# Kernel optimization log

Measured on AMD Instinct MI355X. Metric: run time of the kernel, lower is better.

## Reference

```python
import jax, jax.numpy as jnp
import numpy as np

IN_DIM = 128
LAYER_DIMS = [128, 128]
NUM_SAMPLES = [25, 10]
L0 = 3072
NEG_WEIGHT = 1.0


def setup_inputs() -> dict:
    key = jax.random.key(0)
    ks = jax.random.split(key, 12)
    feat = jax.random.normal(ks[0], (L0, IN_DIM), dtype=jnp.float32)
    nodes = jax.random.randint(ks[1], (L0,), 0, L0)
    nb0 = jnp.arange(L0)
    nb1 = jax.random.randint(ks[2], (L0 * 10,), 0, L0)
    nb2 = jax.random.randint(ks[3], (L0 * 10 * 25,), 0, L0)
    src_idx = jax.random.randint(ks[4], (1024,), 0, L0)
    pos_idx = jax.random.randint(ks[5], (1024,), 0, L0)
    neg_idx = jax.random.randint(ks[6], (512,), 0, L0)
    g = 0.05
    # mean aggregator weights: layer0 in=IN_DIM, layer1 in=2*128 (concat)
    w_self_0 = jax.random.normal(ks[7], (IN_DIM, 128), jnp.float32) * g
    w_neigh_0 = jax.random.normal(ks[8], (IN_DIM, 128), jnp.float32) * g
    w_self_1 = jax.random.normal(ks[9], (256, 128), jnp.float32) * g
    w_neigh_1 = jax.random.normal(ks[10], (256, 128), jnp.float32) * g
    return dict(nodes=nodes, feat=feat, src_idx=src_idx, pos_idx=pos_idx,
                neg_idx=neg_idx, nb0=nb0, nb1=nb1, nb2=nb2,
                w_self_0=w_self_0, w_neigh_0=w_neigh_0,
                w_self_1=w_self_1, w_neigh_1=w_neigh_1)


def _aggregate(hidden, params):
    # GraphSAGE layer stack: at layer l, combine each hop with the mean of its
    # sampled neighbors, concat self/neigh transforms, relu except last layer.
    num_layers = len(NUM_SAMPLES)
    for layer in range(num_layers):
        w_self, w_neigh = params[layer]
        is_last = layer == num_layers - 1
        next_hidden = []
        for hop in range(num_layers - layer):
            s = NUM_SAMPLES[num_layers - hop - 1]
            self_v = hidden[hop]  # [n, d]
            neigh = hidden[hop + 1].reshape(self_v.shape[0], s, self_v.shape[1])
            neigh_mean = jnp.mean(neigh, axis=1)
            h = jnp.concatenate([self_v @ w_self, neigh_mean @ w_neigh], axis=1)
            if not is_last:
                h = jax.nn.relu(h)
            next_hidden.append(h)
        hidden = next_hidden
    return hidden[0]


def _l2_normalize(x, eps=1e-12):
    return x * jax.lax.rsqrt(jnp.maximum(jnp.sum(x * x, axis=1, keepdims=True), eps))


def reference(nodes, feat, src_idx, pos_idx, neg_idx, nb0, nb1, nb2,
              w_self_0, w_neigh_0, w_self_1, w_neigh_1):
    hidden = [feat[nb0], feat[nb1], feat[nb2]]
    params = [(w_self_0, w_neigh_0), (w_self_1, w_neigh_1)]
    output = _aggregate(hidden, params)          # [L0, 256]
    output = _l2_normalize(output)
    src_emb = output[src_idx]                    # [B, 256]
    pos_emb = output[pos_idx]
    neg_emb = output[neg_idx]                    # [Nneg, 256]

    aff = jnp.sum(src_emb * pos_emb, axis=1)     # [B]
    neg_aff = src_emb @ neg_emb.T                # [B, Nneg]

    # MRR via double argsort (tf double top_k equivalent; ties -> positive last)
    aff_all = jnp.concatenate([neg_aff, aff[:, None]], axis=1)
    order = jnp.argsort(-aff_all, axis=1, stable=True)
    ranks = jnp.argsort(order, axis=1, stable=True)
    mrr = jnp.mean(1.0 / (ranks[:, -1].astype(jnp.float32) + 1.0))

    # sigmoid cross-entropy: labels 1 -> softplus(-x); labels 0 -> softplus(x)
    true_xent = jax.nn.softplus(-aff)
    neg_xent = jax.nn.softplus(neg_aff)
    loss = jnp.sum(true_xent) + NEG_WEIGHT * jnp.sum(neg_xent)
    loss = loss / jnp.asarray(src_emb.shape[0], jnp.float32)
    return src_emb, loss, mrr
```

## Files before the change

kernel.cpp:

```cpp
#include <hip/hip_runtime.h>
#include <math.h>

#define L0      3072
#define BATCH   1024
#define NNEG    512
#define LDP     264

typedef __attribute__((ext_vector_type(8))) short bf16x8;
typedef __attribute__((ext_vector_type(4))) float f32x4;


__device__ __forceinline__ float bf2f(unsigned short u) {
  return __uint_as_float(((unsigned)u) << 16);
}
__device__ __forceinline__ void store_out(float v, float* p) { *p = v; }
__device__ __forceinline__ void store_out(float v, unsigned short* p) {
  unsigned x = __float_as_uint(v);
  *p = (unsigned short)((x + 0x7fff + ((x >> 16) & 1)) >> 16);
}

template<int K, int AW, int HOFF, bool NORM, typename OutT>
__global__ __launch_bounds__(512) void k_mm(
    const float* __restrict__ Ain,
    const float* __restrict__ W0, const float* __restrict__ W1,
    OutT* __restrict__ Out, const int ldo, const int outHalfOff,
    unsigned short* __restrict__ OutB,
    float* __restrict__ zbuf, const int zcount) {
  __shared__ float AT[6 * AW];
  __shared__ float rs[8][3];
  const int t = threadIdx.x;
  if (zbuf != nullptr && blockIdx.x == 0)
    for (int z = t; z < zcount; z += 512) zbuf[z] = 0.f;
  const int base = blockIdx.x * 6;
  {
    const float4* __restrict__ src = (const float4*)(Ain + base * AW);
    float4* __restrict__ dst = (float4*)AT;
    for (int idx = t; idx < 6 * AW / 4; idx += 512) dst[idx] = src[idx];
  }
  __syncthreads();

  const int wave = t >> 6;
  const int half = wave >> 2;
  const int colg = (wave >> 1) & 1;
  const int rowg = wave & 1;
  const int rg = rowg * 3;
  const int col = colg * 64 + (t & 63);
  const float* __restrict__ W = (half ? W1 : W0) + col;
  const float* __restrict__ A0 = AT + rg * AW + half * HOFF;

  float acc[3] = {0.f, 0.f, 0.f};
#pragma unroll 4
  for (int d = 0; d < K; d += 4) {
    float4 a[3];
#pragma unroll
    for (int r = 0; r < 3; ++r) a[r] = *(const float4*)&A0[r * AW + d];
    float w[4];
#pragma unroll
    for (int i2 = 0; i2 < 4; ++i2) w[i2] = W[(d + i2) * 128];
#pragma unroll
    for (int i2 = 0; i2 < 4; ++i2)
#pragma unroll
      for (int r = 0; r < 3; ++r)
        acc[r] = fmaf(((const float*)&a[r])[i2], w[i2], acc[r]);
  }

  float scale[3] = {1.f, 1.f, 1.f};
  if (NORM) {
    float p[3];
#pragma unroll
    for (int r = 0; r < 3; ++r) p[r] = acc[r] * acc[r];
#pragma unroll
    for (int off = 32; off > 0; off >>= 1)
#pragma unroll
      for (int r = 0; r < 3; ++r) p[r] += __shfl_xor(p[r], off, 64);
    if ((t & 63) == 0) { rs[wave][0] = p[0]; rs[wave][1] = p[1]; rs[wave][2] = p[2]; }
    __syncthreads();
#pragma unroll
    for (int r = 0; r < 3; ++r) {
      const float s = rs[rowg][r] + rs[rowg + 2][r] + rs[rowg + 4][r] + rs[rowg + 6][r];
      scale[r] = rsqrtf(fmaxf(s, 1e-12f));
    }
  }
  OutT* __restrict__ O = Out + half * outHalfOff;
#pragma unroll
  for (int r = 0; r < 3; ++r) {
    const float v = acc[r] * scale[r];
    store_out(v, &O[(base + rg + r) * ldo + col]);
    if (OutB != nullptr)
      store_out(v, &OutB[(base + rg + r) * 256 + half * 128 + col]);
  }
}

__global__ __launch_bounds__(640) void k_aggregate(
    const unsigned short* __restrict__ X0, const unsigned short* __restrict__ Y0,
    const int* __restrict__ nb0, const int* __restrict__ nb1,
    const int* __restrict__ nb2, float* __restrict__ H) {
  __shared__ float gB[10][128], gC[10][128], gD[10][128];
  const int i = blockIdx.x;
  const int t = threadIdx.x;
  const int n0 = nb0[i];
  const int j = t >> 6;
  const int lam = t & 63;
  const int r = i * 10 + j;
  int myidx = 0;
  if (lam < 25) myidx = nb2[r * 25 + lam];
  else if (lam == 25) myidx = nb1[r];
  const int c8 = lam & 15;
  const int sub = lam >> 4;

  float d8[8];
#pragma unroll
  for (int e = 0; e < 8; ++e) d8[e] = 0.f;
#pragma unroll
  for (int m = 0; m < 7; ++m) {
    const int k = sub + 4 * m;
    const int ridx = __shfl(myidx, k, 64);
    if (k < 25) {
      const float4 raw = *(const float4*)(Y0 + ridx * 128 + c8 * 8);
      const unsigned short* u = (const unsigned short*)&raw;
#pragma unroll
      for (int e = 0; e < 8; ++e) d8[e] += bf2f(u[e]);
    }
  }
#pragma unroll
  for (int e = 0; e < 8; ++e) d8[e] += __shfl_xor(d8[e], 16, 64);
#pragma unroll
  for (int e = 0; e < 8; ++e) d8[e] += __shfl_xor(d8[e], 32, 64);

  const int r1 = __shfl(myidx, 25, 64);
  if (sub == 0) {
#pragma unroll
    for (int e = 0; e < 8; ++e) gD[j][c8 * 8 + e] = fmaxf(d8[e] * 0.04f, 0.f);
    const float4 raw = *(const float4*)(Y0 + r1 * 128 + c8 * 8);
    const unsigned short* u = (const unsigned short*)&raw;
#pragma unroll
    for (int e = 0; e < 8; ++e) gB[j][c8 * 8 + e] = bf2f(u[e]);
  } else if (sub == 1) {
    const float4 raw = *(const float4*)(X0 + r1 * 128 + c8 * 8);
    const unsigned short* u = (const unsigned short*)&raw;
#pragma unroll
    for (int e = 0; e < 8; ++e) gC[j][c8 * 8 + e] = fmaxf(bf2f(u[e]), 0.f);
  }
  __syncthreads();

  if (t < 512) {
    const int q = t >> 7, c = t & 127;
    float v;
    if (q == 0) {
      v = fmaxf(bf2f(X0[n0 * 128 + c]), 0.f);
    } else {
      const float* g = (q == 1) ? &gB[0][0] : (q == 2) ? &gC[0][0] : &gD[0][0];
      float s = 0.f;
#pragma unroll
      for (int jj = 0; jj < 10; ++jj) s += g[jj * 128 + c];
      v = s * 0.1f;
      if (q == 1) v = fmaxf(v, 0.f);
    }
    H[i * 512 + t] = v;
  }
}

__device__ __forceinline__ float softplusf(float x) {
  return fmaxf(x, 0.f) + log1pf(expf(-fabsf(x)));
}

__global__ __launch_bounds__(64) void k_aff(
    const unsigned short* __restrict__ Rb, const float* __restrict__ R,
    const int* __restrict__ src_idx, const int* __restrict__ pos_idx,
    float* __restrict__ out_src, float* __restrict__ aff,
    float* __restrict__ spPos) {
  __shared__ unsigned short Sb[16][LDP];
  __shared__ unsigned short Pb[16][LDP];
  const int t = threadIdx.x;
  const int rowBase = blockIdx.x * 16;
  for (int idx = t; idx < 32 * 32; idx += 64) {
    const int row = idx >> 5, q = idx & 31;
    const int gr = (row < 16) ? src_idx[rowBase + row] : pos_idx[rowBase + row - 16];
    const float4 v = ((const float4*)(Rb + gr * 256))[q];
    unsigned short* dst = (row < 16) ? &Sb[row][0] : &Pb[row - 16][0];
    *(float4*)(dst + q * 8) = v;
  }
  for (int idx = t; idx < 16 * 64; idx += 64) {
    const int row = idx >> 6, q = idx & 63;
    ((float4*)out_src)[(rowBase + row) * 64 + q] =
        ((const float4*)(R + src_idx[rowBase + row] * 256))[q];
  }
  __syncthreads();
  const int lm = t & 15, quad = t >> 4;
  const unsigned short* Sp = &Sb[lm][quad * 8];
  const unsigned short* Pp = &Pb[lm][quad * 8];
  f32x4 d = {0.f, 0.f, 0.f, 0.f};
#pragma unroll
  for (int k0 = 0; k0 < 256; k0 += 32) {
    bf16x8 a = *(const bf16x8*)(Sp + k0);
    bf16x8 b = *(const bf16x8*)(Pp + k0);
    d = __builtin_amdgcn_mfma_f32_16x16x32_bf16(a, b, d, 0, 0, 0);
  }
#pragma unroll
  for (int j = 0; j < 4; ++j) {
    const int row = quad * 4 + j;
    if (lm == row) {
      aff[rowBase + row] = d[j];
      atomicAdd(spPos, softplusf(-d[j]));
    }
  }
}

__global__ __launch_bounds__(256) void k_neg(
    const unsigned short* __restrict__ Rb, const int* __restrict__ src_idx,
    const int* __restrict__ neg_idx, const float* __restrict__ aff,
    int* __restrict__ rank, float* __restrict__ spNeg) {
  __shared__ unsigned short Sb[32][LDP];
  __shared__ unsigned short Nb[64][LDP];
  __shared__ float affL[32];
  const int t = threadIdx.x;
  const int rowBase = (blockIdx.x >> 3) * 32;
  const int colBase = (blockIdx.x & 7) * 64;
  if (t < 32) affL[t] = aff[rowBase + t];
  for (int idx = t; idx < 96 * 32; idx += 256) {
    const int row = idx >> 5, q = idx & 31;
    const int gr = (row < 32) ? src_idx[rowBase + row]
                              : neg_idx[colBase + row - 32];
    const float4 v = ((const float4*)(Rb + gr * 256))[q];
    unsigned short* dst = (row < 32) ? &Sb[row][0] : &Nb[row - 32][0];
    *(float4*)(dst + q * 8) = v;
  }
  __syncthreads();

  const int l = t & 63, w = t >> 6;
  const int mt = w & 1, np = w >> 1;
  const int lm = l & 15, quad = l >> 4;
  const unsigned short* Sp = &Sb[mt * 16 + lm][quad * 8];
  const unsigned short* N0 = &Nb[np * 32 + lm][quad * 8];
  const unsigned short* N1 = &Nb[np * 32 + 16 + lm][quad * 8];
  f32x4 d0 = {0.f, 0.f, 0.f, 0.f}, d1 = {0.f, 0.f, 0.f, 0.f};
#pragma unroll
  for (int k0 = 0; k0 < 256; k0 += 32) {
    bf16x8 a = *(const bf16x8*)(Sp + k0);
    bf16x8 b0 = *(const bf16x8*)(N0 + k0);
    bf16x8 b1 = *(const bf16x8*)(N1 + k0);
    d0 = __builtin_amdgcn_mfma_f32_16x16x32_bf16(a, b0, d0, 0, 0, 0);
    d1 = __builtin_amdgcn_mfma_f32_16x16x32_bf16(a, b1, d1, 0, 0, 0);
  }

  float sp = 0.f;
#pragma unroll
  for (int j = 0; j < 4; ++j) {
    const int row = mt * 16 + quad * 4 + j;
    const float a = affL[row];
    const float v0 = d0[j], v1 = d1[j];
    sp += softplusf(v0) + softplusf(v1);
    int c = (v0 >= a ? 1 : 0) + (v1 >= a ? 1 : 0);
#pragma unroll
    for (int off = 8; off > 0; off >>= 1) c += __shfl_down(c, off, 16);
    if (lm == 0 && c) atomicAdd(&rank[rowBase + row], c);
  }
#pragma unroll
  for (int off = 32; off > 0; off >>= 1) sp += __shfl_down(sp, off, 64);
  if (l == 0) atomicAdd(spNeg, sp);
}

__global__ __launch_bounds__(256) void k_finalize(
    const int* __restrict__ rank, const float* __restrict__ spPos,
    const float* __restrict__ spNeg, float* __restrict__ out) {
  const int t = threadIdx.x;
  float s = 0.f;
  for (int i = t; i < BATCH; i += 256) s += 1.f / (float)(rank[i] + 1);
#pragma unroll
  for (int off = 32; off > 0; off >>= 1) s += __shfl_down(s, off, 64);
  __shared__ float wsum[4];
  if ((t & 63) == 0) wsum[t >> 6] = s;
  __syncthreads();
  if (t == 0) {
    float mrr = (wsum[0] + wsum[1] + wsum[2] + wsum[3]) * (1.f / 1024.f);
    float loss = (spPos[0] + spNeg[0]) * (1.f / 1024.f);
    out[BATCH * 256]     = loss;
    out[BATCH * 256 + 1] = mrr;
  }
}

extern "C" void kernel_launch(void* const* d_in, const int* in_sizes, int n_in,
                              void* d_out, int out_size, void* d_ws, size_t ws_size,
                              hipStream_t stream) {
  const float* feat   = (const float*)d_in[1];
  const int* src_idx  = (const int*)d_in[2];
  const int* pos_idx  = (const int*)d_in[3];
  const int* neg_idx  = (const int*)d_in[4];
  const int* nb0      = (const int*)d_in[5];
  const int* nb1      = (const int*)d_in[6];
  const int* nb2      = (const int*)d_in[7];
  const float* ws0    = (const float*)d_in[8];
  const float* wn0    = (const float*)d_in[9];
  const float* ws1    = (const float*)d_in[10];
  const float* wn1    = (const float*)d_in[11];

  float* wsf = (float*)d_ws;
  unsigned short* X0 = (unsigned short*)d_ws;
  unsigned short* Y0 = X0 + 393216;
  float* H     = wsf + 393216;
  float* R     = wsf + 1966080;
  unsigned short* Rb = (unsigned short*)(wsf + 2752512);
  float* aff   = wsf + 3145728;
  float* spPos = wsf + 3146752;
  float* spNeg = wsf + 3146753;
  int*   rank  = (int*)(wsf + 3146754);
  float* out   = (float*)d_out;

  k_mm<128, 128, 0, false, unsigned short><<<L0 / 6, 512, 0, stream>>>(
      feat, ws0, wn0, X0, 128, 393216, nullptr, spPos, 1026);
  k_aggregate<<<L0, 640, 0, stream>>>(X0, Y0, nb0, nb1, nb2, H);
  k_mm<256, 512, 256, true, float><<<L0 / 6, 512, 0, stream>>>(
      H, ws1, wn1, R, 256, 128, Rb, nullptr, 0);
  k_aff<<<BATCH / 16, 64, 0, stream>>>(Rb, R, src_idx, pos_idx, out, aff, spPos);
  k_neg<<<(BATCH / 32) * (NNEG / 64), 256, 0, stream>>>(
      Rb, src_idx, neg_idx, aff, rank, spNeg);
  k_finalize<<<1, 256, 0, stream>>>(rank, spPos, spNeg, out);
}
```

Measured before the change: 166.2 us.

## Fuse positive affinity and finalize into negative-affinity kernel with last-block reduction

Folds the positive-pair affinity into the negative scoring kernel. Each block computes the src·pos products with an extra MFMA and broadcasts the diagonal by shuffle, and the blocks in the first column also copy the src embeddings to the output. The separate finalize kernel is replaced by an atomic counter, so the last block to finish reduces the ranks and losses. This removes two kernel launches and the aff round-trip through global memory. In exchange, every block recomputes the positive affinities and now loads 32 more rows.

New measurement: 167.5 us. About the same (+0.8%).

```diff
diff --git a/kernel.cpp b/kernel.cpp
--- a/kernel.cpp
+++ b/kernel.cpp
@@ -164,66 +164,37 @@
   return fmaxf(x, 0.f) + log1pf(expf(-fabsf(x)));
 }
 
-__global__ __launch_bounds__(64) void k_aff(
+__global__ __launch_bounds__(256) void k_neg(
     const unsigned short* __restrict__ Rb, const float* __restrict__ R,
     const int* __restrict__ src_idx, const int* __restrict__ pos_idx,
-    float* __restrict__ out_src, float* __restrict__ aff,
-    float* __restrict__ spPos) {
-  __shared__ unsigned short Sb[16][LDP];
-  __shared__ unsigned short Pb[16][LDP];
-  const int t = threadIdx.x;
-  const int rowBase = blockIdx.x * 16;
-  for (int idx = t; idx < 32 * 32; idx += 64) {
-    const int row = idx >> 5, q = idx & 31;
-    const int gr = (row < 16) ? src_idx[rowBase + row] : pos_idx[rowBase + row - 16];
-    const float4 v = ((const float4*)(Rb + gr * 256))[q];
-    unsigned short* dst = (row < 16) ? &Sb[row][0] : &Pb[row - 16][0];
-    *(float4*)(dst + q * 8) = v;
-  }
-  for (int idx = t; idx < 16 * 64; idx += 64) {
-    const int row = idx >> 6, q = idx & 63;
-    ((float4*)out_src)[(rowBase + row) * 64 + q] =
-        ((const float4*)(R + src_idx[rowBase + row] * 256))[q];
-  }
-  __syncthreads();
-  const int lm = t & 15, quad = t >> 4;
-  const unsigned short* Sp = &Sb[lm][quad * 8];
-  const unsigned short* Pp = &Pb[lm][quad * 8];
-  f32x4 d = {0.f, 0.f, 0.f, 0.f};
-#pragma unroll
-  for (int k0 = 0; k0 < 256; k0 += 32) {
-    bf16x8 a = *(const bf16x8*)(Sp + k0);
-    bf16x8 b = *(const bf16x8*)(Pp + k0);
-    d = __builtin_amdgcn_mfma_f32_16x16x32_bf16(a, b, d, 0, 0, 0);
-  }
-#pragma unroll
-  for (int j = 0; j < 4; ++j) {
-    const int row = quad * 4 + j;
-    if (lm == row) {
-      aff[rowBase + row] = d[j];
-      atomicAdd(spPos, softplusf(-d[j]));
-    }
-  }
-}
-
-__global__ __launch_bounds__(256) void k_neg(
-    const unsigned short* __restrict__ Rb, const int* __restrict__ src_idx,
-    const int* __restrict__ neg_idx, const float* __restrict__ aff,
-    int* __restrict__ rank, float* __restrict__ spNeg) {
+    const int* __restrict__ neg_idx, float* __restrict__ out,
+    int* __restrict__ rank, float* __restrict__ spPos,
+    float* __restrict__ spNeg, int* __restrict__ counter) {
   __shared__ unsigned short Sb[32][LDP];
+  __shared__ unsigned short Pb[32][LDP];
   __shared__ unsigned short Nb[64][LDP];
-  __shared__ float affL[32];
+  __shared__ float wsum[4];
+  __shared__ int lastFlag;
   const int t = threadIdx.x;
   const int rowBase = (blockIdx.x >> 3) * 32;
   const int colBase = (blockIdx.x & 7) * 64;
-  if (t < 32) affL[t] = aff[rowBase + t];
-  for (int idx = t; idx < 96 * 32; idx += 256) {
+  const bool first = (colBase == 0);
+
+  for (int idx = t; idx < 128 * 32; idx += 256) {
     const int row = idx >> 5, q = idx & 31;
-    const int gr = (row < 32) ? src_idx[rowBase + row]
-                              : neg_idx[colBase + row - 32];
-    const float4 v = ((const float4*)(Rb + gr * 256))[q];
-    unsigned short* dst = (row < 32) ? &Sb[row][0] : &Nb[row - 32][0];
-    *(float4*)(dst + q * 8) = v;
+    int gr;
+    unsigned short* dst;
+    if (row < 32)      { gr = src_idx[rowBase + row];      dst = &Sb[row][0]; }
+    else if (row < 64) { gr = pos_idx[rowBase + row - 32]; dst = &Pb[row - 32][0]; }
+    else               { gr = neg_idx[colBase + row - 64]; dst = &Nb[row - 64][0]; }
+    *(float4*)(dst + q * 8) = ((const float4*)(Rb + gr * 256))[q];
+  }
+  if (first) {
+    for (int idx = t; idx < 32 * 64; idx += 256) {
+      const int rr = idx >> 6, qq = idx & 63;
+      ((float4*)out)[(rowBase + rr) * 64 + qq] =
+          ((const float4*)R)[src_idx[rowBase + rr] * 64 + qq];
+    }
   }
   __syncthreads();
 
@@ -231,14 +202,18 @@
   const int mt = w & 1, np = w >> 1;
   const int lm = l & 15, quad = l >> 4;
   const unsigned short* Sp = &Sb[mt * 16 + lm][quad * 8];
+  const unsigned short* Pp = &Pb[mt * 16 + lm][quad * 8];
   const unsigned short* N0 = &Nb[np * 32 + lm][quad * 8];
   const unsigned short* N1 = &Nb[np * 32 + 16 + lm][quad * 8];
+  f32x4 da = {0.f, 0.f, 0.f, 0.f};
   f32x4 d0 = {0.f, 0.f, 0.f, 0.f}, d1 = {0.f, 0.f, 0.f, 0.f};
 #pragma unroll
   for (int k0 = 0; k0 < 256; k0 += 32) {
-    bf16x8 a = *(const bf16x8*)(Sp + k0);
+    bf16x8 a  = *(const bf16x8*)(Sp + k0);
+    bf16x8 bp = *(const bf16x8*)(Pp + k0);
     bf16x8 b0 = *(const bf16x8*)(N0 + k0);
     bf16x8 b1 = *(const bf16x8*)(N1 + k0);
+    da = __builtin_amdgcn_mfma_f32_16x16x32_bf16(a, bp, da, 0, 0, 0);
     d0 = __builtin_amdgcn_mfma_f32_16x16x32_bf16(a, b0, d0, 0, 0, 0);
     d1 = __builtin_amdgcn_mfma_f32_16x16x32_bf16(a, b1, d1, 0, 0, 0);
   }
@@ -246,36 +221,42 @@
   float sp = 0.f;
 #pragma unroll
   for (int j = 0; j < 4; ++j) {
-    const int row = mt * 16 + quad * 4 + j;
-    const float a = affL[row];
+    const int rowq = quad * 4 + j;
+    const float av = __shfl(da[j], quad * 20 + j, 64);
+    if (first && np == 0 && lm == rowq)
+      atomicAdd(spPos, softplusf(-da[j]));
     const float v0 = d0[j], v1 = d1[j];
     sp += softplusf(v0) + softplusf(v1);
-    int c = (v0 >= a ? 1 : 0) + (v1 >= a ? 1 : 0);
+    int c = (v0 >= av ? 1 : 0) + (v1 >= av ? 1 : 0);
 #pragma unroll
     for (int off = 8; off > 0; off >>= 1) c += __shfl_down(c, off, 16);
-    if (lm == 0 && c) atomicAdd(&rank[rowBase + row], c);
+    if (lm == 0 && c) atomicAdd(&rank[rowBase + mt * 16 + rowq], c);
   }
 #pragma unroll
   for (int off = 32; off > 0; off >>= 1) sp += __shfl_down(sp, off, 64);
   if (l == 0) atomicAdd(spNeg, sp);
-}
-
-__global__ __launch_bounds__(256) void k_finalize(
-    const int* __restrict__ rank, const float* __restrict__ spPos,
-    const float* __restrict__ spNeg, float* __restrict__ out) {
-  const int t = threadIdx.x;
-  float s = 0.f;
-  for (int i = t; i < BATCH; i += 256) s += 1.f / (float)(rank[i] + 1);
-#pragma unroll
-  for (int off = 32; off > 0; off >>= 1) s += __shfl_down(s, off, 64);
-  __shared__ float wsum[4];
-  if ((t & 63) == 0) wsum[t >> 6] = s;
-  __syncthreads();
-  if (t == 0) {
-    float mrr = (wsum[0] + wsum[1] + wsum[2] + wsum[3]) * (1.f / 1024.f);
-    float loss = (spPos[0] + spNeg[0]) * (1.f / 1024.f);
-    out[BATCH * 256]     = loss;
-    out[BATCH * 256 + 1] = mrr;
+
+  __threadfence();
+  __syncthreads();
+  if (t == 0) lastFlag = (atomicAdd(counter, 1) == 255) ? 1 : 0;
+  __syncthreads();
+  if (lastFlag) {
+    float s = 0.f;
+    for (int i = t; i < BATCH; i += 256) {
+      const int rv = atomicAdd(&rank[i], 0);
+      s += 1.f / (float)(rv + 1);
+    }
+#pragma unroll
+    for (int off = 32; off > 0; off >>= 1) s += __shfl_down(s, off, 64);
+    if ((t & 63) == 0) wsum[t >> 6] = s;
+    __syncthreads();
+    if (t == 0) {
+      const float mrr = (wsum[0] + wsum[1] + wsum[2] + wsum[3]) * (1.f / 1024.f);
+      const float pv = atomicAdd(spPos, 0.f);
+      const float nv = atomicAdd(spNeg, 0.f);
+      out[BATCH * 256]     = (pv + nv) * (1.f / 1024.f);
+      out[BATCH * 256 + 1] = mrr;
+    }
   }
 }
 
@@ -300,19 +281,17 @@
   float* H     = wsf + 393216;
   float* R     = wsf + 1966080;
   unsigned short* Rb = (unsigned short*)(wsf + 2752512);
-  float* aff   = wsf + 3145728;
-  float* spPos = wsf + 3146752;
-  float* spNeg = wsf + 3146753;
-  int*   rank  = (int*)(wsf + 3146754);
+  float* spPos = wsf + 3145728;
+  float* spNeg = wsf + 3145729;
+  int*   rank  = (int*)(wsf + 3145730);
+  int*   counter = (int*)(wsf + 3145730 + 1024);
   float* out   = (float*)d_out;
 
   k_mm<128, 128, 0, false, unsigned short><<<L0 / 6, 512, 0, stream>>>(
-      feat, ws0, wn0, X0, 128, 393216, nullptr, spPos, 1026);
+      feat, ws0, wn0, X0, 128, 393216, nullptr, spPos, 1027);
   k_aggregate<<<L0, 640, 0, stream>>>(X0, Y0, nb0, nb1, nb2, H);
   k_mm<256, 512, 256, true, float><<<L0 / 6, 512, 0, stream>>>(
       H, ws1, wn1, R, 256, 128, Rb, nullptr, 0);
-  k_aff<<<BATCH / 16, 64, 0, stream>>>(Rb, R, src_idx, pos_idx, out, aff, spPos);
   k_neg<<<(BATCH / 32) * (NNEG / 64), 256, 0, stream>>>(
-      Rb, src_idx, neg_idx, aff, rank, spNeg);
-  k_finalize<<<1, 256, 0, stream>>>(rank, spPos, spNeg, out);
-}
+      Rb, R, src_idx, pos_idx, neg_idx, out, rank, spPos, spNeg, counter);
+}
```
